# Optimization experiments

Hardware: AMD Instinct MI355X
Metric: run time of the kernel (lower is better)

## Reference

```python
import jax, jax.numpy as jnp
import numpy as np

N_NODES = 100000
N_EDGES = 1600000
D = 128
LEAKY_SLOPE = 0.01  # torch nn.LeakyReLU default


def setup_inputs() -> dict:
    key = jax.random.key(0)
    k1, k2, k3, k4 = jax.random.split(key, 4)
    in_states = jax.random.normal(k1, (N_NODES, D), dtype=jnp.float32)
    edges = jax.random.randint(k2, (2, N_EDGES), 0, N_NODES, dtype=jnp.int64)
    # Linear weights, kaiming-uniform-ish scale
    W_msg = jax.random.normal(k3, (D, D), dtype=jnp.float32) / np.sqrt(D)
    attn_w = jax.random.normal(k4, (2 * D,), dtype=jnp.float32) / np.sqrt(2 * D)
    W_res = jnp.eye(D, dtype=jnp.float32)  # eye-initialized, frozen residual proj
    passthrough_coef = jnp.ones((1,), dtype=jnp.float32)
    return {"in_states": in_states, "edges": edges, "W_msg": W_msg,
            "attn_w": attn_w, "W_res": W_res, "passthrough_coef": passthrough_coef}


def reference(in_states, edges, W_msg, attn_w, W_res, passthrough_coef):
    n_nodes = in_states.shape[0]
    src, dst = edges[0], edges[1]

    # message transform (dropout in eval mode -> identity)
    messages = in_states @ W_msg.T                       # [N, D]

    # attention score: Linear(2D->1) on cat([m_from, m_to]) == split dot products
    s_from = messages @ attn_w[:D]                       # [N]
    s_to = messages @ attn_w[D:]                         # [N]
    e = s_from[src] + s_to[dst]                          # [E]
    e = jnp.where(e >= 0, e, LEAKY_SLOPE * e)            # LeakyReLU

    # indexed (segment) softmax over destination nodes
    seg_max = jax.ops.segment_max(e, dst, num_segments=n_nodes)
    e_exp = jnp.exp(e - seg_max[dst])
    seg_sum = jax.ops.segment_sum(e_exp, dst, num_segments=n_nodes)
    alpha = e_exp / seg_sum[dst]                         # [E]

    # weighted scatter-add aggregation
    scaled = alpha[:, None] * messages[src]              # [E, D]
    merged = jax.ops.segment_sum(scaled, dst, num_segments=n_nodes)  # [N, D]

    new_states_res = jax.nn.relu(merged)
    old_passthrough = (in_states @ W_res.T) * jax.nn.sigmoid(passthrough_coef[0])
    return old_passthrough + new_states_res
```

## Files before the change

### kernel.cpp

```cpp
#include <hip/hip_runtime.h>
#include <hip/hip_fp16.h>


#define DD 128
#define NPB 32
#define LEAKY 0.01f
#define BSH 3
#define BSZ 8

#define FMA4(A, XS, W)                                        \
  A.x = fmaf((XS), (W).x, A.x); A.y = fmaf((XS), (W).y, A.y); \
  A.z = fmaf((XS), (W).z, A.z); A.w = fmaf((XS), (W).w, A.w)

__global__ void k_transpose2(const float* __restrict__ Wm, const float* __restrict__ Wr,
                             float* __restrict__ WTm, float* __restrict__ WTr) {
  int idx = blockIdx.x * blockDim.x + threadIdx.x;
  if (idx < DD * DD) {
    int j = idx >> 7, k = idx & (DD - 1);
    WTm[k * DD + j] = Wm[idx];
    WTr[k * DD + j] = Wr[idx];
  }
}

__global__ void k_zero(int* __restrict__ p, int n) {
  int i = blockIdx.x * blockDim.x + threadIdx.x;
  if (i < n) p[i] = 0;
}

__global__ void k_detect(const int* __restrict__ e, int* __restrict__ flag) {
  if (threadIdx.x == 0 && blockIdx.x == 0) {
    int all0 = 1;
    for (int i = 0; i < 64; ++i)
      if (e[2 * i + 1] != 0) { all0 = 0; break; }
    flag[0] = all0;
  }
}

__global__ void k_eye(const float* __restrict__ Wr, int* __restrict__ eyeflag) {
  __shared__ int ok_s;
  if (threadIdx.x == 0) ok_s = 1;
  __syncthreads();
  int ok = 1;
  for (int i = threadIdx.x; i < DD * DD; i += 256) {
    float expect = ((i >> 7) == (i & (DD - 1))) ? 1.f : 0.f;
    if (Wr[i] != expect) ok = 0;
  }
  if (!ok) ok_s = 0;
  __syncthreads();
  if (threadIdx.x == 0) eyeflag[0] = ok_s;
}

__global__ __launch_bounds__(256) void k_msg(
    const float* __restrict__ x, const float* __restrict__ WTm,
    const float* __restrict__ WTr, const float* __restrict__ attn_w,
    const float* __restrict__ coef, const int* __restrict__ eyeflag, int n_nodes,
    __half* __restrict__ mh, float* __restrict__ s_from,
    float* __restrict__ s_to, float* __restrict__ out) {
  __shared__ float4 lw4[32 * 32];
  __shared__ float4 lx4[NPB * 32];
  __shared__ float lds_aw[2 * DD];
  const int t = threadIdx.x;
  const int base = blockIdx.x * NPB;
  const int nvalid = min(NPB, n_nodes - base);

  const float4* xs = (const float4*)(x + (size_t)base * DD);
  const int nflt4 = nvalid * 32;
  for (int i = t; i < nflt4; i += 256) lx4[i] = xs[i];
  if (t < 2 * DD) lds_aw[t] = attn_w[t];

  const int j4 = t & 31;
  const int g = t >> 5;
  const int r0 = (g * 4 + 0) * 32, r1 = r0 + 32, r2 = r1 + 32, r3 = r2 + 32;

  float4 a0, a1, a2, a3;

#define GEMM128(WT)                                                           \
  a0 = a1 = a2 = a3 = make_float4(0.f, 0.f, 0.f, 0.f);                        \
  _Pragma("unroll 1")                                                         \
  for (int chunk = 0; chunk < 4; ++chunk) {                                   \
    __syncthreads();                                                          \
    const float4* wsrc = (const float4*)((WT) + chunk * 32 * DD);             \
    lw4[t] = wsrc[t];                                                         \
    lw4[t + 256] = wsrc[t + 256];                                             \
    lw4[t + 512] = wsrc[t + 512];                                             \
    lw4[t + 768] = wsrc[t + 768];                                             \
    __syncthreads();                                                          \
    const int xb = chunk * 8;                                                 \
    _Pragma("unroll 2")                                                       \
    for (int k = 0; k < 32; k += 4) {                                         \
      float4 w0 = lw4[(k + 0) * 32 + j4];                                     \
      float4 w1 = lw4[(k + 1) * 32 + j4];                                     \
      float4 w2 = lw4[(k + 2) * 32 + j4];                                     \
      float4 w3 = lw4[(k + 3) * 32 + j4];                                     \
      float4 x0 = lx4[r0 + xb + (k >> 2)];                                    \
      float4 x1 = lx4[r1 + xb + (k >> 2)];                                    \
      float4 x2 = lx4[r2 + xb + (k >> 2)];                                    \
      float4 x3 = lx4[r3 + xb + (k >> 2)];                                    \
      FMA4(a0, x0.x, w0); FMA4(a0, x0.y, w1);                                 \
      FMA4(a0, x0.z, w2); FMA4(a0, x0.w, w3);                                 \
      FMA4(a1, x1.x, w0); FMA4(a1, x1.y, w1);                                 \
      FMA4(a1, x1.z, w2); FMA4(a1, x1.w, w3);                                 \
      FMA4(a2, x2.x, w0); FMA4(a2, x2.y, w1);                                 \
      FMA4(a2, x2.z, w2); FMA4(a2, x2.w, w3);                                 \
      FMA4(a3, x3.x, w0); FMA4(a3, x3.y, w1);                                 \
      FMA4(a3, x3.z, w2); FMA4(a3, x3.w, w3);                                 \
    }                                                                         \
  }

  GEMM128(WTm);
  {
    float4 av[4] = {a0, a1, a2, a3};
#pragma unroll
    for (int b = 0; b < 4; ++b) {
      int n = g * 4 + b;
      if (n < nvalid) {
        int gn = base + n;
        float4 v = av[b];
        union { __half2 h2[2]; uint2 u; } pk;
        pk.h2[0] = __floats2half2_rn(v.x, v.y);
        pk.h2[1] = __floats2half2_rn(v.z, v.w);
        ((uint2*)(mh + (size_t)gn * DD))[j4] = pk.u;
        float sf = v.x * lds_aw[4 * j4] + v.y * lds_aw[4 * j4 + 1] +
                   v.z * lds_aw[4 * j4 + 2] + v.w * lds_aw[4 * j4 + 3];
        float stv = v.x * lds_aw[DD + 4 * j4] + v.y * lds_aw[DD + 4 * j4 + 1] +
                    v.z * lds_aw[DD + 4 * j4 + 2] + v.w * lds_aw[DD + 4 * j4 + 3];
#pragma unroll
        for (int m = 16; m; m >>= 1) {
          sf += __shfl_xor(sf, m, 32);
          stv += __shfl_xor(stv, m, 32);
        }
        if (j4 == 0) { s_from[gn] = sf; s_to[gn] = stv; }
      }
    }
  }

  const float sig = 1.f / (1.f + __expf(-coef[0]));
  if (eyeflag[0]) {
    float4* od = (float4*)(out + (size_t)base * DD);
    for (int i = t; i < nflt4; i += 256) {
      float4 v = lx4[i];
      v.x *= sig; v.y *= sig; v.z *= sig; v.w *= sig;
      od[i] = v;
    }
  } else {
    GEMM128(WTr);
    float4 av[4] = {a0, a1, a2, a3};
#pragma unroll
    for (int b = 0; b < 4; ++b) {
      int n = g * 4 + b;
      if (n < nvalid) {
        int gn = base + n;
        float4 v = av[b];
        v.x *= sig; v.y *= sig; v.z *= sig; v.w *= sig;
        ((float4*)(out + (size_t)gn * DD))[j4] = v;
      }
    }
  }
#undef GEMM128
}

__global__ void k_bcount(const int* __restrict__ edges, int n_edges, int n_nodes,
                         const int* __restrict__ flag, int* __restrict__ bcnt) {
  int i = blockIdx.x * blockDim.x + threadIdx.x;
  if (i < n_edges) {
    int d = flag[0] ? ((const int2*)edges)[n_edges + i].x : edges[n_edges + i];
    if ((unsigned)d < (unsigned)n_nodes) atomicAdd(&bcnt[d >> BSH], 1);
  }
}

__global__ __launch_bounds__(256) void k_bscan(const int* __restrict__ cnt, int nb,
                                               int* __restrict__ bstart,
                                               int* __restrict__ bcursor) {
  __shared__ int lds[256];
  __shared__ int carry_s;
  const int t = threadIdx.x;
  if (t == 0) carry_s = 0;
  __syncthreads();
  const int nchunks = (nb + 1023) / 1024;
  for (int c = 0; c < nchunks; ++c) {
    const int carry = carry_s;
    const int base = c * 1024 + t * 4;
    int v0 = 0, v1 = 0, v2 = 0, v3 = 0;
    if (base + 0 < nb) v0 = cnt[base + 0];
    if (base + 1 < nb) v1 = cnt[base + 1];
    if (base + 2 < nb) v2 = cnt[base + 2];
    if (base + 3 < nb) v3 = cnt[base + 3];
    const int tsum = v0 + v1 + v2 + v3;
    int val = tsum;
    lds[t] = val;
    __syncthreads();
    for (int off = 1; off < 256; off <<= 1) {
      int a = (t >= off) ? lds[t - off] : 0;
      __syncthreads();
      val += a;
      lds[t] = val;
      __syncthreads();
    }
    int o0 = carry + val - tsum;
    int o1 = o0 + v0, o2 = o1 + v1, o3 = o2 + v2;
    if (base + 0 < nb) { bstart[base + 0] = o0; bcursor[base + 0] = o0; }
    if (base + 1 < nb) { bstart[base + 1] = o1; bcursor[base + 1] = o1; }
    if (base + 2 < nb) { bstart[base + 2] = o2; bcursor[base + 2] = o2; }
    if (base + 3 < nb) { bstart[base + 3] = o3; bcursor[base + 3] = o3; }
    __syncthreads();
    if (t == 255) carry_s = carry + val;
    __syncthreads();
  }
  if (t == 0) bstart[nb] = carry_s;
}

__global__ void k_bscatter(const int* __restrict__ edges, int n_edges, int n_nodes,
                           const int* __restrict__ flag, int* __restrict__ bcursor,
                           int* __restrict__ packed) {
  int i = blockIdx.x * blockDim.x + threadIdx.x;
  if (i < n_edges) {
    int d, s;
    if (flag[0]) {
      d = ((const int2*)edges)[n_edges + i].x;
      s = ((const int2*)edges)[i].x;
    } else {
      d = edges[n_edges + i];
      s = edges[i];
    }
    if ((unsigned)d < (unsigned)n_nodes) {
      if ((unsigned)s >= (unsigned)n_nodes) s = 0;
      int pos = atomicAdd(&bcursor[d >> BSH], 1);
      packed[pos] = (s << BSH) | (d & (BSZ - 1));
    }
  }
}

__global__ __launch_bounds__(256) void k_wagg(
    const int* __restrict__ bstart, const int* __restrict__ packed,
    const float* __restrict__ s_from, const float* __restrict__ s_to,
    const __half* __restrict__ mh, int n_nodes, int nb, float* __restrict__ out) {
  const int lane = threadIdx.x & 63;
  const int b = blockIdx.x * 4 + (threadIdx.x >> 6);
  if (b >= nb) return;
  const int start = bstart[b], end = bstart[b + 1];
  if (start >= end) return;
  const int nbase = b << BSH;

  float ws0 = 0.f, ax0 = 0.f, ay0 = 0.f;
  float ws1 = 0.f, ax1 = 0.f, ay1 = 0.f;
  float ws2 = 0.f, ax2 = 0.f, ay2 = 0.f;
  float ws3 = 0.f, ax3 = 0.f, ay3 = 0.f;
  float ws4 = 0.f, ax4 = 0.f, ay4 = 0.f;
  float ws5 = 0.f, ax5 = 0.f, ay5 = 0.f;
  float ws6 = 0.f, ax6 = 0.f, ay6 = 0.f;
  float ws7 = 0.f, ax7 = 0.f, ay7 = 0.f;

  for (int cb = start; cb < end; cb += 64) {
    const int cnt = min(64, end - cb);
    int u = 0;
    float wv = 0.f;
    if (lane < cnt) {
      u = packed[cb + lane];
      int s = u >> BSH;
      float e = s_from[s] + s_to[nbase + (u & (BSZ - 1))];
      e = (e >= 0.f) ? e : LEAKY * e;
      wv = __expf(e);
    }
#pragma unroll 4
    for (int i = 0; i < cnt; ++i) {
      int ui = __shfl(u, i, 64);
      float wi = __shfl(wv, i, 64);
      const float2 mf =
          __half22float2(((const __half2*)(mh + (size_t)(ui >> BSH) * DD))[lane]);
      const int dl = __builtin_amdgcn_readfirstlane(ui) & (BSZ - 1);
      if (dl == 0)      { ws0 += wi; ax0 = fmaf(wi, mf.x, ax0); ay0 = fmaf(wi, mf.y, ay0); }
      else if (dl == 1) { ws1 += wi; ax1 = fmaf(wi, mf.x, ax1); ay1 = fmaf(wi, mf.y, ay1); }
      else if (dl == 2) { ws2 += wi; ax2 = fmaf(wi, mf.x, ax2); ay2 = fmaf(wi, mf.y, ay2); }
      else if (dl == 3) { ws3 += wi; ax3 = fmaf(wi, mf.x, ax3); ay3 = fmaf(wi, mf.y, ay3); }
      else if (dl == 4) { ws4 += wi; ax4 = fmaf(wi, mf.x, ax4); ay4 = fmaf(wi, mf.y, ay4); }
      else if (dl == 5) { ws5 += wi; ax5 = fmaf(wi, mf.x, ax5); ay5 = fmaf(wi, mf.y, ay5); }
      else if (dl == 6) { ws6 += wi; ax6 = fmaf(wi, mf.x, ax6); ay6 = fmaf(wi, mf.y, ay6); }
      else              { ws7 += wi; ax7 = fmaf(wi, mf.x, ax7); ay7 = fmaf(wi, mf.y, ay7); }
    }
  }

#define EPI(K)                                                                \
  {                                                                           \
    int node = nbase + K;                                                     \
    if (node < n_nodes && ws##K > 0.f) {                                      \
      float inv = 1.f / ws##K;                                                \
      float axx = ax##K * inv, ayy = ay##K * inv;                             \
      axx = axx > 0.f ? axx : 0.f;                                            \
      ayy = ayy > 0.f ? ayy : 0.f;                                            \
      float2* orow = (float2*)(out + (size_t)node * DD);                      \
      float2 po = orow[lane];                                                 \
      orow[lane] = make_float2(po.x + axx, po.y + ayy);                       \
    }                                                                         \
  }
  EPI(0) EPI(1) EPI(2) EPI(3) EPI(4) EPI(5) EPI(6) EPI(7)
#undef EPI
}

extern "C" void kernel_launch(void* const* d_in, const int* in_sizes, int n_in,
                              void* d_out, int out_size, void* d_ws, size_t ws_size,
                              hipStream_t stream) {
  const float* x = (const float*)d_in[0];
  const int* edges = (const int*)d_in[1];
  const float* Wm = (const float*)d_in[2];
  const float* aw = (const float*)d_in[3];
  const float* Wr = (const float*)d_in[4];
  const float* coef = (const float*)d_in[5];
  float* out = (float*)d_out;

  const int N = in_sizes[0] / DD;
  const int E = in_sizes[1] / 2;
  const int nb = (N + BSZ - 1) / BSZ;

  const size_t need = ((size_t)N * DD * 2 + 256)
                    + 2 * ((size_t)N * 4 + 256)
                    + 2 * ((size_t)DD * DD * 4 + 256)
                    + 3 * ((size_t)(nb + 1) * 4 + 512)
                    + 1024
                    + (size_t)E * 4 + 256;
  if (ws_size < need) return;

  char* w = (char*)d_ws;
  auto alloc = [&](size_t bytes) {
    char* p = w;
    w += (bytes + 255) & ~(size_t)255;
    return p;
  };
  __half* mh     = (__half*)alloc((size_t)N * DD * 2);
  float* s_from  = (float*)alloc((size_t)N * 4);
  float* s_to    = (float*)alloc((size_t)N * 4);
  float* WTm     = (float*)alloc((size_t)DD * DD * 4);
  float* WTr     = (float*)alloc((size_t)DD * DD * 4);
  int*   bcnt    = (int*)alloc((size_t)nb * 4);
  int*   bstart  = (int*)alloc((size_t)(nb + 1) * 4);
  int*   bcursor = (int*)alloc((size_t)nb * 4);
  int*   flag    = (int*)alloc(256);
  int*   packed  = (int*)alloc((size_t)E * 4);

  k_detect<<<1, 64, 0, stream>>>(edges, flag);
  k_eye<<<1, 256, 0, stream>>>(Wr, flag + 1);
  k_transpose2<<<(DD * DD + 255) / 256, 256, 0, stream>>>(Wm, Wr, WTm, WTr);
  k_zero<<<(nb + 255) / 256, 256, 0, stream>>>(bcnt, nb);
  k_msg<<<(N + NPB - 1) / NPB, 256, 0, stream>>>(x, WTm, WTr, aw, coef, flag + 1,
                                                 N, mh, s_from, s_to, out);
  k_bcount<<<(E + 255) / 256, 256, 0, stream>>>(edges, E, N, flag, bcnt);
  k_bscan<<<1, 256, 0, stream>>>(bcnt, nb, bstart, bcursor);
  k_bscatter<<<(E + 255) / 256, 256, 0, stream>>>(edges, E, N, flag, bcursor, packed);
  k_wagg<<<(nb + 3) / 4, 256, 0, stream>>>(bstart, packed, s_from, s_to,
                                           mh, N, nb, out);
}
```

Before: 494.7 us.

## Sort bucketed edges into per-node CSR and aggregate one wave per node

Adds a wave-level ballot/popcount counting sort that turns the 8-node buckets into a per-destination CSR (`row_start` plus `srcs`). Aggregation then uses one wavefront per node with a single accumulator pair, instead of one wave per bucket with eight accumulator sets and a per-edge uniform branch. The goal is more parallelism, lower register pressure and no per-edge bucket dispatch. The cost is an extra kernel plus another read and write of the edge array. Each wave now handles only about 16 edges, so the per-chunk weight computation leaves most lanes idle.

```diff
diff --git a/kernel.cpp b/kernel.cpp
--- a/kernel.cpp
+++ b/kernel.cpp
@@ -230,70 +230,125 @@
   }
 }
 
-__global__ __launch_bounds__(256) void k_wagg(
+__global__ __launch_bounds__(256) void k_bsort(
     const int* __restrict__ bstart, const int* __restrict__ packed,
-    const float* __restrict__ s_from, const float* __restrict__ s_to,
-    const __half* __restrict__ mh, int n_nodes, int nb, float* __restrict__ out) {
+    int nb, int n_nodes, int n_edges_total,
+    int* __restrict__ srcs, int* __restrict__ row_start) {
   const int lane = threadIdx.x & 63;
   const int b = blockIdx.x * 4 + (threadIdx.x >> 6);
   if (b >= nb) return;
   const int start = bstart[b], end = bstart[b + 1];
+  const int nbase = b << BSH;
+  if (b == 0 && lane == 0) row_start[n_nodes] = n_edges_total;
+
+  int c0 = 0, c1 = 0, c2 = 0, c3 = 0, c4 = 0, c5 = 0, c6 = 0, c7 = 0;
+  for (int cb = start; cb < end; cb += 64) {
+    const bool act = (cb + lane) < end;
+    const int u = act ? packed[cb + lane] : 0;
+    const int dl = u & (BSZ - 1);
+    const unsigned long long b0 = __ballot(act && (dl & 1));
+    const unsigned long long b1 = __ballot(act && (dl & 2));
+    const unsigned long long b2 = __ballot(act && (dl & 4));
+    const unsigned long long ba = __ballot(act);
+    c0 += __popcll(~b0 & ~b1 & ~b2 & ba);
+    c1 += __popcll( b0 & ~b1 & ~b2 & ba);
+    c2 += __popcll(~b0 &  b1 & ~b2 & ba);
+    c3 += __popcll( b0 &  b1 & ~b2 & ba);
+    c4 += __popcll(~b0 & ~b1 &  b2 & ba);
+    c5 += __popcll( b0 & ~b1 &  b2 & ba);
+    c6 += __popcll(~b0 &  b1 &  b2 & ba);
+    c7 += __popcll( b0 &  b1 &  b2 & ba);
+  }
+  const int o0 = 0, o1 = o0 + c0, o2 = o1 + c1, o3 = o2 + c2, o4 = o3 + c3,
+            o5 = o4 + c4, o6 = o5 + c5, o7 = o6 + c6;
+  if (lane == 0) {
+    if (nbase + 0 < n_nodes) row_start[nbase + 0] = start + o0;
+    if (nbase + 1 < n_nodes) row_start[nbase + 1] = start + o1;
+    if (nbase + 2 < n_nodes) row_start[nbase + 2] = start + o2;
+    if (nbase + 3 < n_nodes) row_start[nbase + 3] = start + o3;
+    if (nbase + 4 < n_nodes) row_start[nbase + 4] = start + o4;
+    if (nbase + 5 < n_nodes) row_start[nbase + 5] = start + o5;
+    if (nbase + 6 < n_nodes) row_start[nbase + 6] = start + o6;
+    if (nbase + 7 < n_nodes) row_start[nbase + 7] = start + o7;
+  }
+  int r0 = o0, r1 = o1, r2 = o2, r3 = o3, r4 = o4, r5 = o5, r6 = o6, r7 = o7;
+  for (int cb = start; cb < end; cb += 64) {
+    const bool act = (cb + lane) < end;
+    const int u = act ? packed[cb + lane] : 0;
+    const int dl = u & (BSZ - 1);
+    const unsigned long long b0 = __ballot(act && (dl & 1));
+    const unsigned long long b1 = __ballot(act && (dl & 2));
+    const unsigned long long b2 = __ballot(act && (dl & 4));
+    const unsigned long long ba = __ballot(act);
+    const unsigned long long m0 = (dl & 1) ? b0 : ~b0;
+    const unsigned long long m1 = (dl & 2) ? b1 : ~b1;
+    const unsigned long long m2 = (dl & 4) ? b2 : ~b2;
+    const unsigned long long mymask = m0 & m1 & m2 & ba;
+    const int rank = __popcll(mymask & ((1ull << lane) - 1ull));
+    int basep = r0;
+    basep = (dl == 1) ? r1 : basep;
+    basep = (dl == 2) ? r2 : basep;
+    basep = (dl == 3) ? r3 : basep;
+    basep = (dl == 4) ? r4 : basep;
+    basep = (dl == 5) ? r5 : basep;
+    basep = (dl == 6) ? r6 : basep;
+    basep = (dl == 7) ? r7 : basep;
+    if (act) srcs[start + basep + rank] = u >> BSH;
+    r0 += __popcll(~b0 & ~b1 & ~b2 & ba);
+    r1 += __popcll( b0 & ~b1 & ~b2 & ba);
+    r2 += __popcll(~b0 &  b1 & ~b2 & ba);
+    r3 += __popcll( b0 &  b1 & ~b2 & ba);
+    r4 += __popcll(~b0 & ~b1 &  b2 & ba);
+    r5 += __popcll( b0 & ~b1 &  b2 & ba);
+    r6 += __popcll(~b0 &  b1 &  b2 & ba);
+    r7 += __popcll( b0 &  b1 &  b2 & ba);
+  }
+}
+
+__global__ __launch_bounds__(256) void k_nagg(
+    const int* __restrict__ row_start, const int* __restrict__ srcs,
+    const float* __restrict__ s_from, const float* __restrict__ s_to,
+    const __half* __restrict__ mh, int n_nodes, float* __restrict__ out) {
+  const int lane = threadIdx.x & 63;
+  const int v = blockIdx.x * 4 + (threadIdx.x >> 6);
+  if (v >= n_nodes) return;
+  const int start = row_start[v];
+  const int end = row_start[v + 1];
   if (start >= end) return;
-  const int nbase = b << BSH;
-
-  float ws0 = 0.f, ax0 = 0.f, ay0 = 0.f;
-  float ws1 = 0.f, ax1 = 0.f, ay1 = 0.f;
-  float ws2 = 0.f, ax2 = 0.f, ay2 = 0.f;
-  float ws3 = 0.f, ax3 = 0.f, ay3 = 0.f;
-  float ws4 = 0.f, ax4 = 0.f, ay4 = 0.f;
-  float ws5 = 0.f, ax5 = 0.f, ay5 = 0.f;
-  float ws6 = 0.f, ax6 = 0.f, ay6 = 0.f;
-  float ws7 = 0.f, ax7 = 0.f, ay7 = 0.f;
-
-  for (int cb = start; cb < end; cb += 64) {
-    const int cnt = min(64, end - cb);
-    int u = 0;
-    float wv = 0.f;
+  const float st = s_to[v];
+
+  float wsum = 0.f;
+  float ax = 0.f, ay = 0.f;
+  for (int cbase = start; cbase < end; cbase += 64) {
+    const int cnt = min(64, end - cbase);
+    int s = 0;
+    float w = 0.f;
     if (lane < cnt) {
-      u = packed[cb + lane];
-      int s = u >> BSH;
-      float e = s_from[s] + s_to[nbase + (u & (BSZ - 1))];
-      e = (e >= 0.f) ? e : LEAKY * e;
-      wv = __expf(e);
-    }
-#pragma unroll 4
+      s = srcs[cbase + lane];
+      float xx = s_from[s] + st;
+      xx = (xx >= 0.f) ? xx : LEAKY * xx;
+      w = __expf(xx);
+    }
+    wsum += w;
+#pragma unroll 8
     for (int i = 0; i < cnt; ++i) {
-      int ui = __shfl(u, i, 64);
-      float wi = __shfl(wv, i, 64);
+      int si = __shfl(s, i, 64);
+      float wi = __shfl(w, i, 64);
       const float2 mf =
-          __half22float2(((const __half2*)(mh + (size_t)(ui >> BSH) * DD))[lane]);
-      const int dl = __builtin_amdgcn_readfirstlane(ui) & (BSZ - 1);
-      if (dl == 0)      { ws0 += wi; ax0 = fmaf(wi, mf.x, ax0); ay0 = fmaf(wi, mf.y, ay0); }
-      else if (dl == 1) { ws1 += wi; ax1 = fmaf(wi, mf.x, ax1); ay1 = fmaf(wi, mf.y, ay1); }
-      else if (dl == 2) { ws2 += wi; ax2 = fmaf(wi, mf.x, ax2); ay2 = fmaf(wi, mf.y, ay2); }
-      else if (dl == 3) { ws3 += wi; ax3 = fmaf(wi, mf.x, ax3); ay3 = fmaf(wi, mf.y, ay3); }
-      else if (dl == 4) { ws4 += wi; ax4 = fmaf(wi, mf.x, ax4); ay4 = fmaf(wi, mf.y, ay4); }
-      else if (dl == 5) { ws5 += wi; ax5 = fmaf(wi, mf.x, ax5); ay5 = fmaf(wi, mf.y, ay5); }
-      else if (dl == 6) { ws6 += wi; ax6 = fmaf(wi, mf.x, ax6); ay6 = fmaf(wi, mf.y, ay6); }
-      else              { ws7 += wi; ax7 = fmaf(wi, mf.x, ax7); ay7 = fmaf(wi, mf.y, ay7); }
-    }
-  }
-
-#define EPI(K)                                                                \
-  {                                                                           \
-    int node = nbase + K;                                                     \
-    if (node < n_nodes && ws##K > 0.f) {                                      \
-      float inv = 1.f / ws##K;                                                \
-      float axx = ax##K * inv, ayy = ay##K * inv;                             \
-      axx = axx > 0.f ? axx : 0.f;                                            \
-      ayy = ayy > 0.f ? ayy : 0.f;                                            \
-      float2* orow = (float2*)(out + (size_t)node * DD);                      \
-      float2 po = orow[lane];                                                 \
-      orow[lane] = make_float2(po.x + axx, po.y + ayy);                       \
-    }                                                                         \
-  }
-  EPI(0) EPI(1) EPI(2) EPI(3) EPI(4) EPI(5) EPI(6) EPI(7)
-#undef EPI
+          __half22float2(((const __half2*)(mh + (size_t)si * DD))[lane]);
+      ax = fmaf(wi, mf.x, ax);
+      ay = fmaf(wi, mf.y, ay);
+    }
+  }
+#pragma unroll
+  for (int m = 32; m; m >>= 1) wsum += __shfl_xor(wsum, m, 64);
+  const float inv = 1.f / wsum;
+  ax *= inv; ay *= inv;
+  ax = (ax > 0.f) ? ax : 0.f;
+  ay = (ay > 0.f) ? ay : 0.f;
+  float2* orow = (float2*)(out + (size_t)v * DD);
+  float2 po = orow[lane];
+  orow[lane] = make_float2(po.x + ax, po.y + ay);
 }
 
 extern "C" void kernel_launch(void* const* d_in, const int* in_sizes, int n_in,
@@ -315,8 +370,9 @@
                     + 2 * ((size_t)N * 4 + 256)
                     + 2 * ((size_t)DD * DD * 4 + 256)
                     + 3 * ((size_t)(nb + 1) * 4 + 512)
+                    + ((size_t)(N + 1) * 4 + 256)
                     + 1024
-                    + (size_t)E * 4 + 256;
+                    + 2 * ((size_t)E * 4 + 256);
   if (ws_size < need) return;
 
   char* w = (char*)d_ws;
@@ -333,8 +389,10 @@
   int*   bcnt    = (int*)alloc((size_t)nb * 4);
   int*   bstart  = (int*)alloc((size_t)(nb + 1) * 4);
   int*   bcursor = (int*)alloc((size_t)nb * 4);
+  int*   row_start = (int*)alloc((size_t)(N + 1) * 4);
   int*   flag    = (int*)alloc(256);
   int*   packed  = (int*)alloc((size_t)E * 4);
+  int*   srcs    = (int*)alloc((size_t)E * 4);
 
   k_detect<<<1, 64, 0, stream>>>(edges, flag);
   k_eye<<<1, 256, 0, stream>>>(Wr, flag + 1);
@@ -345,6 +403,8 @@
   k_bcount<<<(E + 255) / 256, 256, 0, stream>>>(edges, E, N, flag, bcnt);
   k_bscan<<<1, 256, 0, stream>>>(bcnt, nb, bstart, bcursor);
   k_bscatter<<<(E + 255) / 256, 256, 0, stream>>>(edges, E, N, flag, bcursor, packed);
-  k_wagg<<<(nb + 3) / 4, 256, 0, stream>>>(bstart, packed, s_from, s_to,
-                                           mh, N, nb, out);
-}
+  k_bsort<<<(nb + 3) / 4, 256, 0, stream>>>(bstart, packed, nb, N, E,
+                                            srcs, row_start);
+  k_nagg<<<(N + 3) / 4, 256, 0, stream>>>(row_start, srcs, s_from, s_to,
+                                          mh, N, out);
+}
```

After: 476.7 us. -3.6%, faster.
